# Optimization experiments

Measured on AMD Instinct MI355X. Metric: run time of the kernel, lower is better.

The kernel has to match this reference:

```python
import jax, jax.numpy as jnp
import numpy as np

B, N, D, H = 2048, 512, 128, 256
TRADE_K, N_BEST, CONF_TH = 10, 50, 0.05


def setup_inputs() -> dict:
    key = jax.random.key(0)
    ks = jax.random.split(key, 5)
    return {
        "signal_features": jax.random.normal(ks[0], (B, N, D), jnp.float32),
        "spread": jax.random.uniform(ks[1], (B, N), jnp.float32, minval=1e-4, maxval=0.01),
        "volatility": jax.random.uniform(ks[2], (B, N), jnp.float32, minval=1e-4, maxval=0.05),
        "W1": jax.random.normal(ks[3], (D, H), jnp.float32) / np.sqrt(D).astype(np.float32),
        "b1": jnp.zeros((H,), jnp.float32),
        "W2": jax.random.normal(ks[4], (H, 1), jnp.float32) / np.sqrt(H).astype(np.float32),
        "b2": jnp.zeros((1,), jnp.float32),
    }


def _scatter_mask(idx, n):
    # idx: [B, k] int32 -> bool mask [B, n] with True at idx positions
    b = idx.shape[0]
    return jnp.zeros((b, n), bool).at[jnp.arange(b)[:, None], idx].set(True)


def reference(signal_features, spread, volatility, W1, b1, W2, b2):
    # signal predictor: per-asset MLP with sigmoid head -> [B, N]
    h = jax.nn.relu(jnp.einsum('bnd,dh->bnh', signal_features, W1) + b1)
    signal_repr = jax.nn.sigmoid(jnp.einsum('bnh,ho->bno', h, W2)[..., 0] + b2[0])
    ls_score = signal_repr - 0.5  # allow_short_positions=True

    n_best = min(N_BEST, N)
    valid_spread = jnp.isfinite(spread) & (spread > 0)
    ratio = jnp.where(valid_spread, volatility / (spread + 1e-8), -jnp.inf)
    _, best_idx = jax.lax.top_k(ratio, n_best)
    universe_mask = _scatter_mask(best_idx, N)
    # rows with no valid spread: whole universe allowed
    universe_mask = universe_mask | ~valid_spread.any(axis=1, keepdims=True)

    masked_abs = jnp.where(universe_mask, jnp.abs(ls_score), -jnp.inf)
    k = min(TRADE_K, n_best)
    _, top_idx = jax.lax.top_k(masked_abs, k)
    mask = _scatter_mask(top_idx, N)

    selected = jnp.where(mask, ls_score, 0.0)
    action = selected / (jnp.sum(jnp.abs(selected), axis=1, keepdims=True) + 1e-8)

    confidence = masked_abs.max(axis=1)
    confidence = jnp.where(jnp.isfinite(confidence), confidence, 0.0)
    take_trade = (confidence >= CONF_TH).astype(action.dtype)[:, None]
    action = action * take_trade
    return action, confidence
```

## Files before the change

kernel.cpp:

```cpp
#include <hip/hip_runtime.h>
#include <hip/hip_bf16.h>
#include <math.h>

#define B_ 2048
#define N_ 512
#define D_ 128
#define H_ 256
#define BANDf 2e-4f

typedef __attribute__((ext_vector_type(8))) short bf16x8;
typedef __attribute__((ext_vector_type(4))) float f32x4;

__device__ __forceinline__ short f2bf(float x) {
    unsigned u = __float_as_uint(x);
    u = u + 0x7fffu + ((u >> 16) & 1u);
    return (short)(u >> 16);
}
__device__ __forceinline__ float bf2f(short h) {
    return __uint_as_float(((unsigned)(unsigned short)h) << 16);
}
__device__ __forceinline__ unsigned cvt_pk_bf16(float a, float b) {
    unsigned r;
    asm("v_cvt_pk_bf16_f32 %0, %1, %2" : "=v"(r) : "v"(a), "v"(b));
    return r;
}
template<int K>
__device__ __forceinline__ float dpp_shr_add(float zz) {
    int s = __builtin_amdgcn_update_dpp(0, __float_as_int(zz), 0x110 | K, 0xf, 0xf, true);
    return zz + __int_as_float(s);
}

__global__ __launch_bounds__(256) void pack_w(const float* __restrict__ W1,
                                              short* __restrict__ WpH,
                                              short* __restrict__ WpL)
{
    int tid = blockIdx.x * 256 + threadIdx.x;
    int l  = tid & 63;
    int ks = (tid >> 6) & 3;
    int nf = tid >> 8;
    int n  = nf * 16 + (l & 15);
    int kb = ks * 32 + ((l >> 4) << 3);
    bf16x8 hi, lo;
    #pragma unroll
    for (int j = 0; j < 8; ++j) {
        float w = W1[(size_t)(kb + j) * H_ + n];
        short h = f2bf(w);
        hi[j] = h;
        lo[j] = f2bf(w - bf2f(h));
    }
    *(bf16x8*)&WpH[(size_t)tid * 8] = hi;
    *(bf16x8*)&WpL[(size_t)tid * 8] = lo;
}

__global__ __launch_bounds__(256, 2) void mlp_mfma(
    const float* __restrict__ X, const short* __restrict__ WpH,
    const short* __restrict__ WpL, const float* __restrict__ b1,
    const float* __restrict__ W2, const float* __restrict__ b2,
    float* __restrict__ ls)
{
    __shared__ short Xh[64 * 128];
    __shared__ short Xl[64 * 128];
    __shared__ float zl[256];

    const int t    = threadIdx.x;
    const int lane = t & 63;
    const int wn   = t >> 6;
    const size_t m0 = (size_t)blockIdx.x * 64;

    const bf16x8* WH = (const bf16x8*)WpH;
    const bf16x8* WL = (const bf16x8*)WpL;

    bf16x8 Bhi[4][4];
    #pragma unroll
    for (int q = 0; q < 4; ++q)
        #pragma unroll
        for (int ks = 0; ks < 4; ++ks)
            Bhi[q][ks] = WH[((wn * 4 + q) * 4 + ks) * 64 + lane];

    {
        const float4* Xg = (const float4*)(X + m0 * D_);
        #pragma unroll
        for (int i = 0; i < 8; ++i) {
            int f = t + i * 256;
            float4 v = Xg[f];
            int row = f >> 5, k0 = (f & 31) << 2;
            unsigned h01 = cvt_pk_bf16(v.x, v.y);
            unsigned h23 = cvt_pk_bf16(v.z, v.w);
            float l0 = v.x - __uint_as_float(h01 << 16);
            float l1 = v.y - __uint_as_float(h01 & 0xffff0000u);
            float l2 = v.z - __uint_as_float(h23 << 16);
            float l3 = v.w - __uint_as_float(h23 & 0xffff0000u);
            unsigned lo01 = cvt_pk_bf16(l0, l1);
            unsigned lo23 = cvt_pk_bf16(l2, l3);
            int sidx = (row * 128 + k0) ^ ((row & 7) << 3);
            *(uint2*)&Xh[sidx] = make_uint2(h01, h23);
            *(uint2*)&Xl[sidx] = make_uint2(lo01, lo23);
        }
    }
    __syncthreads();

    f32x4 acc[4][4];
    #pragma unroll
    for (int mf = 0; mf < 4; ++mf)
        #pragma unroll
        for (int q = 0; q < 4; ++q)
            acc[mf][q] = (f32x4){0.f, 0.f, 0.f, 0.f};

    #pragma unroll
    for (int ks = 0; ks < 4; ++ks) {
        bf16x8 Blo[4];
        #pragma unroll
        for (int q = 0; q < 4; ++q)
            Blo[q] = WL[((wn * 4 + q) * 4 + ks) * 64 + lane];
        #pragma unroll
        for (int mf = 0; mf < 4; ++mf) {
            int r = mf * 16 + (lane & 15);
            int sidx = (r * 128 + ks * 32 + ((lane >> 4) << 3)) ^ ((r & 7) << 3);
            bf16x8 Ah = *(const bf16x8*)&Xh[sidx];
            bf16x8 Al = *(const bf16x8*)&Xl[sidx];
            #pragma unroll
            for (int q = 0; q < 4; ++q) {
                acc[mf][q] = __builtin_amdgcn_mfma_f32_16x16x32_bf16(Ah, Bhi[q][ks], acc[mf][q], 0, 0, 0);
                acc[mf][q] = __builtin_amdgcn_mfma_f32_16x16x32_bf16(Al, Bhi[q][ks], acc[mf][q], 0, 0, 0);
                acc[mf][q] = __builtin_amdgcn_mfma_f32_16x16x32_bf16(Ah, Blo[q],     acc[mf][q], 0, 0, 0);
            }
        }
    }

    float b1v[4], w2v[4];
    #pragma unroll
    for (int q = 0; q < 4; ++q) {
        int c = wn * 64 + q * 16 + (lane & 15);
        b1v[q] = b1[c];
        w2v[q] = W2[c];
    }
    #pragma unroll
    for (int mf = 0; mf < 4; ++mf) {
        #pragma unroll
        for (int i = 0; i < 4; ++i) {
            float zz = 0.f;
            #pragma unroll
            for (int q = 0; q < 4; ++q) {
                float h = acc[mf][q][i] + b1v[q];
                h = h > 0.f ? h : 0.f;
                zz += h * w2v[q];
            }
            zz = dpp_shr_add<1>(zz);
            zz = dpp_shr_add<2>(zz);
            zz = dpp_shr_add<4>(zz);
            zz = dpp_shr_add<8>(zz);
            if ((lane & 15) == 15) zl[wn * 64 + mf * 16 + ((lane >> 4) << 2) + i] = zz;
        }
    }
    __syncthreads();
    if (t < 64) {
        float z = zl[t] + zl[64 + t] + zl[128 + t] + zl[192 + t] + b2[0];
        ls[m0 + t] = 1.f / (1.f + expf(-z)) - 0.5f;
    }
}

__device__ __forceinline__ unsigned f2key(float f) {
    unsigned u = __float_as_uint(f);
    return (u & 0x80000000u) ? ~u : (u | 0x80000000u);
}
__device__ __forceinline__ float key2f(unsigned k) {
    return __uint_as_float((k & 0x80000000u) ? (k & 0x7fffffffu) : ~k);
}
__device__ __forceinline__ int lane_lt_count(unsigned long long m) {
    return __builtin_amdgcn_mbcnt_hi((unsigned)(m >> 32),
           __builtin_amdgcn_mbcnt_lo((unsigned)m, 0));
}

__device__ __forceinline__ void radix_topk(const unsigned (&key)[8], int k,
                                           unsigned &T, int &need)
{
    unsigned prefix = 0, maskhi = 0;
    int kk = k;
    for (int bit = 31; bit >= 0; --bit) {
        unsigned b = 1u << bit;
        int cnt1 = 0;
        #pragma unroll
        for (int j = 0; j < 8; ++j) {
            bool one = ((key[j] & maskhi) == prefix) && (key[j] & b);
            cnt1 += __popcll(__ballot(one));
        }
        if (cnt1 >= kk) prefix |= b; else kk -= cnt1;
        maskhi |= b;
    }
    T = prefix; need = kk;
}

__device__ __forceinline__ void tie_member(const unsigned (&key)[8], unsigned T,
                                           int need, bool (&mem)[8])
{
    int base = 0;
    #pragma unroll
    for (int j = 0; j < 8; ++j) {
        unsigned long long eb = __ballot(key[j] == T);
        int r = base + lane_lt_count(eb);
        mem[j] = (key[j] > T) || ((key[j] == T) && (r < need));
        base += __popcll(eb);
    }
}

__global__ __launch_bounds__(256) void select_kernel(
    const float* __restrict__ ls, const float* __restrict__ spread,
    const float* __restrict__ vol, const float* __restrict__ X,
    const float* __restrict__ W1, const float* __restrict__ b1,
    const float* __restrict__ W2, const float* __restrict__ b2,
    float* __restrict__ action, float* __restrict__ conf_out)
{
    const int t = threadIdx.x;
    const int l = t & 63;
    const int w = t >> 6;
    const int b = blockIdx.x * 4 + w;
    const size_t base = (size_t)b * N_;

    float rv[8], lsv[8];
    unsigned kr[8];
    bool anyv = false;
    #pragma unroll
    for (int j = 0; j < 8; ++j) {
        int n = l + (j << 6);
        float sp = spread[base + n];
        float vo = vol[base + n];
        bool valid = isfinite(sp) && (sp > 0.f);
        rv[j]  = valid ? (vo / (sp + 1e-8f)) : -INFINITY;
        lsv[j] = ls[base + n];
        anyv |= valid;
        kr[j] = f2key(rv[j]);
    }
    bool allow_all = (__any((int)anyv) == 0);

    unsigned T50; int need50;
    radix_topk(kr, 50, T50, need50);
    bool mem50[8];
    tie_member(kr, T50, need50, mem50);

    float mabs[8];
    unsigned km[8];
    #pragma unroll
    for (int j = 0; j < 8; ++j) {
        bool u = allow_all || mem50[j];
        mabs[j] = u ? fabsf(lsv[j]) : -INFINITY;
        km[j] = f2key(mabs[j]);
    }
    unsigned T10; int need10;
    radix_topk(km, 10, T10, need10);
    bool mem10[8];
    tie_member(km, T10, need10, mem10);
    float b10 = key2f(T10);

    float zp = 0.f, cf = -INFINITY;
    #pragma unroll
    for (int j = 0; j < 8; ++j) {
        if (mem10[j]) zp += mabs[j];
        cf = fmaxf(cf, mabs[j]);
    }
    #pragma unroll
    for (int s = 1; s < 64; s <<= 1) {
        zp += __shfl_xor(zp, s, 64);
        cf = fmaxf(cf, __shfl_xor(cf, s, 64));
    }
    float conf = cf;

    bool confclose = fabsf(conf - 0.05f) <= BANDf;
    bool inband[8];
    int nb = 0;
    #pragma unroll
    for (int j = 0; j < 8; ++j) {
        inband[j] = (mabs[j] != -INFINITY) && (fabsf(mabs[j] - b10) <= BANDf);
        nb += __popcll(__ballot(inband[j]));
    }
    bool redo = (nb >= 2) || confclose;

    if (!redo) {
        float cfin  = isfinite(conf) ? conf : 0.f;
        float scale = (cfin >= 0.05f) ? (1.f / (zp + 1e-8f)) : 0.f;
        #pragma unroll
        for (int j = 0; j < 8; ++j) {
            int n = l + (j << 6);
            action[base + n] = mem10[j] ? lsv[j] * scale : 0.f;
        }
        if (l == 0) conf_out[b] = cfin;
        return;
    }

    const float2* xr2 = (const float2*)&X[base * D_];
    float4 bb = *(const float4*)&b1[l * 4];
    float4 ww = *(const float4*)&W2[l * 4];
    const float b2v = b2[0];

    #pragma unroll
    for (int j = 0; j < 8; ++j) {
        bool cand = (nb >= 2 && inband[j]) || (confclose && mabs[j] == conf);
        unsigned long long bal = __ballot(cand);
        while (bal) {
            int s = __ffsll((long long)bal) - 1;
            bal &= bal - 1;
            int asset = s + (j << 6);
            float2 x2 = xr2[(size_t)asset * 64 + l];
            float h0 = 0.f, h1 = 0.f, h2 = 0.f, h3 = 0.f;
            #pragma unroll 16
            for (int kk = 0; kk < D_; ++kk) {
                float xk = __shfl((kk & 1) ? x2.y : x2.x, kk >> 1, 64);
                float4 wv = *(const float4*)&W1[(size_t)kk * H_ + l * 4];
                h0 += xk * wv.x; h1 += xk * wv.y; h2 += xk * wv.z; h3 += xk * wv.w;
            }
            h0 += bb.x; h1 += bb.y; h2 += bb.z; h3 += bb.w;
            float zz = (h0 > 0.f ? h0 : 0.f) * ww.x + (h1 > 0.f ? h1 : 0.f) * ww.y
                     + (h2 > 0.f ? h2 : 0.f) * ww.z + (h3 > 0.f ? h3 : 0.f) * ww.w;
            #pragma unroll
            for (int sh = 1; sh < 64; sh <<= 1) zz += __shfl_xor(zz, sh, 64);
            float val = 1.f / (1.f + expf(-(zz + b2v))) - 0.5f;
            if (l == s) {
                lsv[j]  = val;
                mabs[j] = fabsf(val);
                km[j]   = f2key(mabs[j]);
            }
        }
    }

    unsigned T10b; int need10b;
    radix_topk(km, 10, T10b, need10b);
    bool mem10b[8];
    tie_member(km, T10b, need10b, mem10b);

    float zx = 0.f, cfx = -INFINITY;
    #pragma unroll
    for (int j = 0; j < 8; ++j) {
        if (mem10b[j]) zx += mabs[j];
        cfx = fmaxf(cfx, mabs[j]);
    }
    #pragma unroll
    for (int s = 1; s < 64; s <<= 1) {
        zx += __shfl_xor(zx, s, 64);
        cfx = fmaxf(cfx, __shfl_xor(cfx, s, 64));
    }
    cfx = isfinite(cfx) ? cfx : 0.f;
    float scale = (cfx >= 0.05f) ? (1.f / (zx + 1e-8f)) : 0.f;
    #pragma unroll
    for (int j = 0; j < 8; ++j) {
        int n = l + (j << 6);
        action[base + n] = mem10b[j] ? lsv[j] * scale : 0.f;
    }
    if (l == 0) conf_out[b] = cfx;
}

extern "C" void kernel_launch(void* const* d_in, const int* in_sizes, int n_in,
                              void* d_out, int out_size, void* d_ws, size_t ws_size,
                              hipStream_t stream)
{
    const float* X  = (const float*)d_in[0];
    const float* sp = (const float*)d_in[1];
    const float* vo = (const float*)d_in[2];
    const float* W1 = (const float*)d_in[3];
    const float* b1 = (const float*)d_in[4];
    const float* W2 = (const float*)d_in[5];
    const float* b2 = (const float*)d_in[6];

    float* action = (float*)d_out;
    float* conf   = action + (size_t)B_ * N_;

    float* ls = (float*)d_ws;
    size_t need = (size_t)B_ * N_ * 4 + 2 * (size_t)D_ * H_ * 2;
    short *WpH, *WpL;
    if (ws_size >= need) {
        WpH = (short*)((char*)d_ws + (size_t)B_ * N_ * 4);
        WpL = WpH + (size_t)D_ * H_;
    } else {
        WpH = (short*)(action + (size_t)out_size - 2 * (size_t)D_ * H_ / 2);
        WpL = WpH + (size_t)D_ * H_;
    }

    hipLaunchKernelGGL(pack_w, dim3(16), dim3(256), 0, stream, W1, WpH, WpL);
    hipLaunchKernelGGL(mlp_mfma, dim3((B_ * N_) / 64), dim3(256), 0, stream,
                       X, WpH, WpL, b1, W2, b2, ls);
    hipLaunchKernelGGL(select_kernel, dim3(B_ / 4), dim3(256), 0, stream,
                       ls, sp, vo, X, W1, b1, W2, b2, action, conf);
}
```

Before: 284.6 us.

## Make MLP kernel persistent with double-buffered async global-to-LDS loads

Turns the MLP kernel into a persistent grid of 768 blocks, each looping over 32-row tiles. The next tile is prefetched straight into a double-buffered fp32 LDS tile with global_load_lds while the current one is computed. The bf16 hi/lo split now happens at fragment-read time instead of being stored to LDS. The aim is to hide HBM latency for the 128 MB input stream and raise occupancy to 3 blocks per CU. The cost is more LDS read traffic (fp32), conversion work repeated across the four waves, and tail handling of the sigmoid writes.

Result: slower. 489.8 us (+72.1%).

```diff
diff --git a/kernel.cpp b/kernel.cpp
--- a/kernel.cpp
+++ b/kernel.cpp
@@ -7,6 +7,8 @@
 #define D_ 128
 #define H_ 256
 #define BANDf 2e-4f
+#define TILE_R 32
+#define GRID_MLP 768
 
 typedef __attribute__((ext_vector_type(8))) short bf16x8;
 typedef __attribute__((ext_vector_type(4))) float f32x4;
@@ -28,6 +30,11 @@
 __device__ __forceinline__ float dpp_shr_add(float zz) {
     int s = __builtin_amdgcn_update_dpp(0, __float_as_int(zz), 0x110 | K, 0xf, 0xf, true);
     return zz + __int_as_float(s);
+}
+__device__ __forceinline__ void gld_lds16(const float* g, float* l) {
+    __builtin_amdgcn_global_load_lds(
+        (const __attribute__((address_space(1))) void*)g,
+        (__attribute__((address_space(3))) void*)l, 16, 0, 0);
 }
 
 __global__ __launch_bounds__(256) void pack_w(const float* __restrict__ W1,
@@ -52,20 +59,18 @@
     *(bf16x8*)&WpL[(size_t)tid * 8] = lo;
 }
 
-__global__ __launch_bounds__(256, 2) void mlp_mfma(
+__global__ __launch_bounds__(256, 3) void mlp_mfma(
     const float* __restrict__ X, const short* __restrict__ WpH,
     const short* __restrict__ WpL, const float* __restrict__ b1,
     const float* __restrict__ W2, const float* __restrict__ b2,
     float* __restrict__ ls)
 {
-    __shared__ short Xh[64 * 128];
-    __shared__ short Xl[64 * 128];
-    __shared__ float zl[256];
+    __shared__ float Xf[2][TILE_R * 128];
+    __shared__ float zl[2][128];
 
     const int t    = threadIdx.x;
     const int lane = t & 63;
     const int wn   = t >> 6;
-    const size_t m0 = (size_t)blockIdx.x * 64;
 
     const bf16x8* WH = (const bf16x8*)WpH;
     const bf16x8* WL = (const bf16x8*)WpL;
@@ -76,56 +81,6 @@
         #pragma unroll
         for (int ks = 0; ks < 4; ++ks)
             Bhi[q][ks] = WH[((wn * 4 + q) * 4 + ks) * 64 + lane];
-
-    {
-        const float4* Xg = (const float4*)(X + m0 * D_);
-        #pragma unroll
-        for (int i = 0; i < 8; ++i) {
-            int f = t + i * 256;
-            float4 v = Xg[f];
-            int row = f >> 5, k0 = (f & 31) << 2;
-            unsigned h01 = cvt_pk_bf16(v.x, v.y);
-            unsigned h23 = cvt_pk_bf16(v.z, v.w);
-            float l0 = v.x - __uint_as_float(h01 << 16);
-            float l1 = v.y - __uint_as_float(h01 & 0xffff0000u);
-            float l2 = v.z - __uint_as_float(h23 << 16);
-            float l3 = v.w - __uint_as_float(h23 & 0xffff0000u);
-            unsigned lo01 = cvt_pk_bf16(l0, l1);
-            unsigned lo23 = cvt_pk_bf16(l2, l3);
-            int sidx = (row * 128 + k0) ^ ((row & 7) << 3);
-            *(uint2*)&Xh[sidx] = make_uint2(h01, h23);
-            *(uint2*)&Xl[sidx] = make_uint2(lo01, lo23);
-        }
-    }
-    __syncthreads();
-
-    f32x4 acc[4][4];
-    #pragma unroll
-    for (int mf = 0; mf < 4; ++mf)
-        #pragma unroll
-        for (int q = 0; q < 4; ++q)
-            acc[mf][q] = (f32x4){0.f, 0.f, 0.f, 0.f};
-
-    #pragma unroll
-    for (int ks = 0; ks < 4; ++ks) {
-        bf16x8 Blo[4];
-        #pragma unroll
-        for (int q = 0; q < 4; ++q)
-            Blo[q] = WL[((wn * 4 + q) * 4 + ks) * 64 + lane];
-        #pragma unroll
-        for (int mf = 0; mf < 4; ++mf) {
-            int r = mf * 16 + (lane & 15);
-            int sidx = (r * 128 + ks * 32 + ((lane >> 4) << 3)) ^ ((r & 7) << 3);
-            bf16x8 Ah = *(const bf16x8*)&Xh[sidx];
-            bf16x8 Al = *(const bf16x8*)&Xl[sidx];
-            #pragma unroll
-            for (int q = 0; q < 4; ++q) {
-                acc[mf][q] = __builtin_amdgcn_mfma_f32_16x16x32_bf16(Ah, Bhi[q][ks], acc[mf][q], 0, 0, 0);
-                acc[mf][q] = __builtin_amdgcn_mfma_f32_16x16x32_bf16(Al, Bhi[q][ks], acc[mf][q], 0, 0, 0);
-                acc[mf][q] = __builtin_amdgcn_mfma_f32_16x16x32_bf16(Ah, Blo[q],     acc[mf][q], 0, 0, 0);
-            }
-        }
-    }
 
     float b1v[4], w2v[4];
     #pragma unroll
@@ -134,28 +89,114 @@
         b1v[q] = b1[c];
         w2v[q] = W2[c];
     }
-    #pragma unroll
-    for (int mf = 0; mf < 4; ++mf) {
-        #pragma unroll
-        for (int i = 0; i < 4; ++i) {
-            float zz = 0.f;
+    const float b2v = b2[0];
+
+    const int NTILES = (B_ * N_) / TILE_R;
+
+    auto stage = [&](int tt, int nb) {
+        const float* src = X + (size_t)tt * TILE_R * 128;
+        #pragma unroll
+        for (int j = 0; j < 4; ++j) {
+            int g = wn * 4 + j;
+            int r = g * 2 + (lane >> 5);
+            int c = (lane & 31) ^ (r & 7);
+            gld_lds16(src + r * 128 + c * 4, &Xf[nb][g * 256]);
+        }
+    };
+
+    int tile = blockIdx.x;
+    if (tile < NTILES) stage(tile, 0);
+    __syncthreads();
+
+    int it = 0;
+    size_t m_prev = 0;
+
+    for (; tile < NTILES; tile += GRID_MLP, ++it) {
+        const int cur = it & 1, nxt = cur ^ 1;
+
+        if (tile + GRID_MLP < NTILES) stage(tile + GRID_MLP, nxt);
+        __builtin_amdgcn_sched_barrier(0);
+
+        if (it > 0 && t < TILE_R) {
+            float z = zl[nxt][t] + zl[nxt][32 + t] + zl[nxt][64 + t] + zl[nxt][96 + t] + b2v;
+            ls[m_prev + t] = 1.f / (1.f + expf(-z)) - 0.5f;
+        }
+
+        f32x4 acc[2][4];
+        #pragma unroll
+        for (int mf = 0; mf < 2; ++mf)
             #pragma unroll
-            for (int q = 0; q < 4; ++q) {
-                float h = acc[mf][q][i] + b1v[q];
-                h = h > 0.f ? h : 0.f;
-                zz += h * w2v[q];
+            for (int q = 0; q < 4; ++q)
+                acc[mf][q] = (f32x4){0.f, 0.f, 0.f, 0.f};
+
+        #pragma unroll
+        for (int ks = 0; ks < 4; ++ks) {
+            bf16x8 Blo[4];
+            #pragma unroll
+            for (int q = 0; q < 4; ++q)
+                Blo[q] = WL[((wn * 4 + q) * 4 + ks) * 64 + lane];
+            #pragma unroll
+            for (int mf = 0; mf < 2; ++mf) {
+                int r  = mf * 16 + (lane & 15);
+                int k0 = ks * 32 + ((lane >> 4) << 3);
+                int sw = (r & 7) << 2;
+                f32x4 v0 = *(const f32x4*)&Xf[cur][r * 128 + (k0 ^ sw)];
+                f32x4 v1 = *(const f32x4*)&Xf[cur][r * 128 + ((k0 + 4) ^ sw)];
+                union { unsigned u[4]; bf16x8 v; } Ah, Al;
+                Ah.u[0] = cvt_pk_bf16(v0[0], v0[1]);
+                Ah.u[1] = cvt_pk_bf16(v0[2], v0[3]);
+                Ah.u[2] = cvt_pk_bf16(v1[0], v1[1]);
+                Ah.u[3] = cvt_pk_bf16(v1[2], v1[3]);
+                float l0 = v0[0] - __uint_as_float(Ah.u[0] << 16);
+                float l1 = v0[1] - __uint_as_float(Ah.u[0] & 0xffff0000u);
+                float l2 = v0[2] - __uint_as_float(Ah.u[1] << 16);
+                float l3 = v0[3] - __uint_as_float(Ah.u[1] & 0xffff0000u);
+                float l4 = v1[0] - __uint_as_float(Ah.u[2] << 16);
+                float l5 = v1[1] - __uint_as_float(Ah.u[2] & 0xffff0000u);
+                float l6 = v1[2] - __uint_as_float(Ah.u[3] << 16);
+                float l7 = v1[3] - __uint_as_float(Ah.u[3] & 0xffff0000u);
+                Al.u[0] = cvt_pk_bf16(l0, l1);
+                Al.u[1] = cvt_pk_bf16(l2, l3);
+                Al.u[2] = cvt_pk_bf16(l4, l5);
+                Al.u[3] = cvt_pk_bf16(l6, l7);
+                #pragma unroll
+                for (int q = 0; q < 4; ++q) {
+                    acc[mf][q] = __builtin_amdgcn_mfma_f32_16x16x32_bf16(Ah.v, Bhi[q][ks], acc[mf][q], 0, 0, 0);
+                    acc[mf][q] = __builtin_amdgcn_mfma_f32_16x16x32_bf16(Al.v, Bhi[q][ks], acc[mf][q], 0, 0, 0);
+                    acc[mf][q] = __builtin_amdgcn_mfma_f32_16x16x32_bf16(Ah.v, Blo[q],     acc[mf][q], 0, 0, 0);
+                }
             }
-            zz = dpp_shr_add<1>(zz);
-            zz = dpp_shr_add<2>(zz);
-            zz = dpp_shr_add<4>(zz);
-            zz = dpp_shr_add<8>(zz);
-            if ((lane & 15) == 15) zl[wn * 64 + mf * 16 + ((lane >> 4) << 2) + i] = zz;
-        }
-    }
-    __syncthreads();
-    if (t < 64) {
-        float z = zl[t] + zl[64 + t] + zl[128 + t] + zl[192 + t] + b2[0];
-        ls[m0 + t] = 1.f / (1.f + expf(-z)) - 0.5f;
+        }
+
+        #pragma unroll
+        for (int mf = 0; mf < 2; ++mf) {
+            #pragma unroll
+            for (int i = 0; i < 4; ++i) {
+                float zz = 0.f;
+                #pragma unroll
+                for (int q = 0; q < 4; ++q) {
+                    float h = acc[mf][q][i] + b1v[q];
+                    h = h > 0.f ? h : 0.f;
+                    zz += h * w2v[q];
+                }
+                zz = dpp_shr_add<1>(zz);
+                zz = dpp_shr_add<2>(zz);
+                zz = dpp_shr_add<4>(zz);
+                zz = dpp_shr_add<8>(zz);
+                if ((lane & 15) == 15)
+                    zl[cur][wn * 32 + mf * 16 + ((lane >> 4) << 2) + i] = zz;
+            }
+        }
+
+        m_prev = (size_t)tile * TILE_R;
+
+        __syncthreads();
+    }
+
+    if (it > 0 && t < TILE_R) {
+        const int lastb = (it - 1) & 1;
+        float z = zl[lastb][t] + zl[lastb][32 + t] + zl[lastb][64 + t] + zl[lastb][96 + t] + b2v;
+        ls[m_prev + t] = 1.f / (1.f + expf(-z)) - 0.5f;
     }
 }
 
@@ -374,7 +415,7 @@
     }
 
     hipLaunchKernelGGL(pack_w, dim3(16), dim3(256), 0, stream, W1, WpH, WpL);
-    hipLaunchKernelGGL(mlp_mfma, dim3((B_ * N_) / 64), dim3(256), 0, stream,
+    hipLaunchKernelGGL(mlp_mfma, dim3(GRID_MLP), dim3(256), 0, stream,
                        X, WpH, WpL, b1, W2, b2, ls);
     hipLaunchKernelGGL(select_kernel, dim3(B_ / 4), dim3(256), 0, stream,
                        ls, sp, vo, X, W1, b1, W2, b2, action, conf);
```
